# Optimization experiments

Hardware: AMD Instinct MI355X
Metric: run time of the kernel (lower is better)

The kernel has to match this reference:

```python
import math
import jax, jax.numpy as jnp
import numpy as np


def _cirlen(scale):
    # replicates UpSample.get_cirlen: smallest rational period of the scale
    for i in (10, 100, 1000, 10000):
        y = scale * i
        x = i
        if y == math.floor(y):
            break
    y = int(round(y))
    g = math.gcd(x, y)
    return y // g


def _proj(out_len, scale, scale_int, in_len):
    # replicates matmask_made: for each output coord, source coord and repeat index (sca),
    # giving the selected column p = coord*scale_int + sca in the nearest-repeated grid.
    c = np.arange(out_len, dtype=np.float64)
    c[-1] -= 0.1
    coord = np.floor(c / scale).astype(np.int64)
    sca = np.arange(out_len) - np.searchsorted(coord, coord)  # occurrence index per coord
    p = coord * scale_int + sca
    # unfold(kernel=3, dilation=2, padding=2): taps at p-2, p, p+2 in the upscaled grid
    q = p[:, None] + 2 * np.array([-1, 0, 1], dtype=np.int64)[None, :]
    valid = ((q >= 0) & (q < in_len * scale_int)).astype(np.float32)
    src = np.clip(q // scale_int, 0, in_len - 1)  # upscaled pixel q == original pixel q//scale_int
    return src, valid


def reference(x, w1, b1, w2, b2, ln_g, ln_b, scale_x10):
    scale = round(scale_x10 / 10.0, 4)
    scale_int = math.ceil(scale)
    N, C, H, W = x.shape
    outH = math.ceil(scale * H)
    outW = math.ceil(scale * W)
    cycle = _cirlen(scale)
    K = 9 * C

    # ---- per-cycle-position dynamic weights (Scale2Pos_mat + Fea2Weight + LayerNorm) ----
    off = np.arange(cycle, dtype=np.float64) / scale
    off = (off - np.floor(off)).astype(np.float32)
    oh_i, ow_j = np.meshgrid(off, off, indexing='ij')  # row index = i*cycle + j
    posmat = np.stack([np.full_like(oh_i, 1.0 / scale), oh_i, ow_j], axis=-1).reshape(-1, 3)
    posmat = jnp.asarray(posmat)
    h = jax.nn.relu(posmat @ w1 + b1)                       # (cyc^2, 256)
    wflat = h @ w2 + b2                                     # (cyc^2, 9*C*outC)
    outC = wflat.shape[-1] // K
    wv = wflat.reshape(cycle * cycle, outC, K)              # view(pos, outC, K)
    mu = wv.mean(-1, keepdims=True)
    var = wv.var(-1, keepdims=True)                         # biased, as torch LayerNorm
    wv = ((wv - mu) / jnp.sqrt(var + 1e-5)) * ln_g + ln_b
    wv = wv / C
    Wm = jnp.transpose(wv, (0, 2, 1)).reshape(cycle, cycle, K, outC)

    # ---- irregular gather (nearest-repeat + unfold + mask_select), done as direct gather ----
    rs, vh = _proj(outH, scale, scale_int, H)  # (outH,3)
    cs, vw = _proj(outW, scale, scale_int, W)  # (outW,3)
    g = x[:, :, jnp.asarray(rs), :]            # (N,C,outH,3,W)
    g = g[:, :, :, :, jnp.asarray(cs)]         # (N,C,outH,3,outW,3)
    g = g * jnp.asarray(vh)[None, None, :, :, None, None]
    g = g * jnp.asarray(vw)[None, None, None, None, :, :]
    # unfold channel order is (C, kh, kw)
    patch = jnp.transpose(g, (0, 2, 4, 1, 3, 5)).reshape(N, outH, outW, K)

    # ---- pad to cycle multiple, per-cycle-position matmul, crop ----
    Hp = -(-outH // cycle) * cycle
    Wp = -(-outW // cycle) * cycle
    patch = jnp.pad(patch, ((0, 0), (0, Hp - outH), (0, Wp - outW), (0, 0)))
    patch = patch.reshape(N, Hp // cycle, cycle, Wp // cycle, cycle, K)
    out = jnp.einsum('nhiwjk,ijkc->nchiwj', patch, Wm)
    out = out.reshape(N, outC, Hp, Wp)[:, :, :outH, :outW]
    return out


def setup_inputs() -> dict:
    key = jax.random.key(0)
    k = jax.random.split(key, 5)
    inC, outC = 64, 3
    x = jax.random.normal(k[0], (8, inC, 96, 96), dtype=jnp.float32)
    w1 = jax.random.normal(k[1], (3, 256), dtype=jnp.float32) * 0.5
    b1 = jax.random.normal(k[2], (256,), dtype=jnp.float32) * 0.1
    w2 = jax.random.normal(k[3], (256, 9 * inC * outC), dtype=jnp.float32) * 0.0625
    b2 = jax.random.normal(k[4], (9 * inC * outC,), dtype=jnp.float32) * 0.01
    ln_g = jnp.ones((9 * inC,), dtype=jnp.float32)
    ln_b = jnp.zeros((9 * inC,), dtype=jnp.float32)
    return {"x": x, "w1": w1, "b1": b1, "w2": w2, "b2": b2,
            "ln_g": ln_g, "ln_b": ln_b, "scale_x10": 15}
```

## Files before the change

### kernel.cpp

```cpp
#include <hip/hip_runtime.h>
#include <math.h>

#define C_IN   64
#define HW_IN  96
#define N_B    8
#define OUTC   3
#define OUT_HW 144
#define HID    256
#define KDIM   576
#define NFLAT  1728

typedef __attribute__((ext_vector_type(8))) short short8;
typedef __attribute__((ext_vector_type(4))) float f32x4;

#define XP_BYTES   (8u * 98 * 98 * 64 * 2)
#define WP_OFF     XP_BYTES
#define WF_OFF     (WP_OFF + 9 * 9216 * 2)
#define WS_NEED    (WF_OFF + NFLAT * 9 * 4)

#define WS_W    0
#define WS_RS   15552
#define WS_VH   15984
#define WS_WF   16416

__device__ __forceinline__ short f2bf(float f) {
    unsigned u = __float_as_uint(f);
    u += 0x7FFFu + ((u >> 16) & 1u);
    return (short)(u >> 16);
}

__global__ __launch_bounds__(256) void a1_wflat(
    const float* __restrict__ w1, const float* __restrict__ b1,
    const float* __restrict__ w2, const float* __restrict__ b2,
    const int* __restrict__ sxp, float* __restrict__ wf)
{
    __shared__ float h[HID];
    __shared__ float part[4 * 64];
    const int cell = blockIdx.x;
    const int tile = blockIdx.y;
    const int tid  = threadIdx.x;

    double scale = (double)sxp[0] / 10.0;
    int ci = cell / 3, cj = cell % 3;
    double oi = (double)ci / scale; oi -= floor(oi);
    double oj = (double)cj / scale; oj -= floor(oj);
    float p0 = (float)(1.0 / scale), p1 = (float)oi, p2 = (float)oj;

    float hv = b1[tid] + p0 * w1[tid] + p1 * w1[HID + tid] + p2 * w1[2 * HID + tid];
    h[tid] = fmaxf(hv, 0.f);
    __syncthreads();

    const int wave = tid >> 6, lane = tid & 63;
    const int col  = tile * 64 + lane;
    const float* w2c = w2 + (size_t)(wave * 64) * NFLAT + col;
    const float* hp  = h + wave * 64;
    float v = 0.f;
    #pragma unroll
    for (int r = 0; r < 64; ++r) v += hp[r] * w2c[(size_t)r * NFLAT];
    part[wave * 64 + lane] = v;
    __syncthreads();

    if (tid < 64) {
        int c2 = tile * 64 + tid;
        float s = b2[c2] + part[tid] + part[64 + tid] + part[128 + tid] + part[192 + tid];
        wf[cell * NFLAT + c2] = s;
    }
}

__global__ __launch_bounds__(128) void prep_xp(
    const float* __restrict__ x, short* __restrict__ xp)
{
    const int n = blockIdx.x, rp = blockIdx.y, sp = threadIdx.x;
    if (sp >= 98) return;
    short8* dst = (short8*)(xp + (((size_t)n * 98 + rp) * 98 + sp) * 64);
    const bool border = (rp == 0) | (rp == 97) | (sp == 0) | (sp == 97);
    if (border) {
        short8 z = {0, 0, 0, 0, 0, 0, 0, 0};
        #pragma unroll
        for (int q = 0; q < 8; ++q) dst[q] = z;
    } else {
        const float* xs = x + (size_t)n * C_IN * 9216 + (rp - 1) * 96 + (sp - 1);
        #pragma unroll
        for (int q = 0; q < 8; ++q) {
            short8 v;
            #pragma unroll
            for (int e = 0; e < 8; ++e)
                v[e] = f2bf(xs[(size_t)(q * 8 + e) * 9216]);
            dst[q] = v;
        }
    }
}

__global__ __launch_bounds__(256) void a2_lnW(
    const float* __restrict__ ln_g, const float* __restrict__ ln_b,
    const float* __restrict__ wf, short* __restrict__ Wp)
{
    __shared__ float rsum[4], rsum2[4];
    const int cell = blockIdx.x, co = blockIdx.y, tid = threadIdx.x;
    const int lane = tid & 63, wid = tid >> 6;

    const float* wfc = wf + cell * NFLAT + co * KDIM;

    float s = 0.f, s2 = 0.f;
    for (int k = tid; k < KDIM; k += 256) { float v = wfc[k]; s += v; s2 += v * v; }
    #pragma unroll
    for (int off = 32; off > 0; off >>= 1) { s += __shfl_down(s, off); s2 += __shfl_down(s2, off); }
    if (lane == 0) { rsum[wid] = s; rsum2[wid] = s2; }
    __syncthreads();
    float S  = rsum[0] + rsum[1] + rsum[2] + rsum[3];
    float Q  = rsum2[0] + rsum2[1] + rsum2[2] + rsum2[3];
    float mu = S * (1.f / KDIM);
    float rstd = rsqrtf(Q * (1.f / KDIM) - mu * mu + 1e-5f);

    for (int k = tid; k < KDIM; k += 256) {
        float v = ((wfc[k] - mu) * rstd * ln_g[k] + ln_b[k]) * (1.f / C_IN);
        int c = k / 9, t = k - 9 * c;
        int kp = t * 64 + c;
        Wp[((size_t)(cell * 72 + (kp >> 3)) * 16 + co) * 8 + (kp & 7)] = f2bf(v);
    }
    if (co == 0) {
        for (int e = tid; e < 72 * 13 * 8; e += 256) {
            int u = e & 7, r = e >> 3;
            int colz = 3 + (r % 13), kc = r / 13;
            Wp[((size_t)(cell * 72 + kc) * 16 + colz) * 8 + u] = 0;
        }
    }
}

__global__ __launch_bounds__(256) void c_mfma(
    const short* __restrict__ xp, const short* __restrict__ Wp,
    float* __restrict__ out)
{
    __shared__ short Bs[9216];
    const int tid = threadIdx.x;
    const int phase = blockIdx.y;
    const int i = phase / 3, jj = phase % 3;

    {
        short8* d = (short8*)Bs;
        const short8* sgl = (const short8*)(Wp + (size_t)phase * 9216);
        for (int e = tid; e < 1152; e += 256) d[e] = sgl[e];
    }
    __syncthreads();

    const int lane = tid & 63, wave = tid >> 6;
    const int q = lane >> 4;

    const int pix = blockIdx.x * 64 + wave * 16;
    const int m0 = pix % 48;
    const int t2 = pix / 48;
    const int k  = t2 % 48;
    const int n  = t2 / 48;

    const int di = (i == 2), dj = (jj == 2);
    const int r0 = 2 * k + di;
    const int m  = m0 + (lane & 15);
    const int s0 = 2 * m + dj;

    const short8* A0 = (const short8*)(xp + (((size_t)n * 98 + r0) * 98 + s0) * 64 + q * 8);
    const short8* A1 = A0 + 98 * 8;
    const short8* A2 = A0 + 196 * 8;
    const short8* Bp = (const short8*)Bs + (q * 16 + (lane & 15));

    f32x4 acc = {0.f, 0.f, 0.f, 0.f};
    #pragma unroll
    for (int kb = 0; kb < 18; ++kb) {
        const int t = kb >> 1, dr = t / 3, dc = t % 3;
        short8 av = (dr == 0 ? A0 : dr == 1 ? A1 : A2)[dc * 8 + (kb & 1) * 4];
        short8 bv = Bp[kb * 64];
        acc = __builtin_amdgcn_mfma_f32_16x16x32_bf16(av, bv, acc, 0, 0, 0);
    }

    const int col = lane & 15;
    if (col < 3) {
        const int oh = i + 3 * k;
        const size_t ob = ((size_t)(n * OUTC + col) * OUT_HW + oh) * OUT_HW;
        #pragma unroll
        for (int reg = 0; reg < 4; ++reg) {
            int mm = m0 + q * 4 + reg;
            out[ob + jj + 3 * mm] = acc[reg];
        }
    }
}

__global__ __launch_bounds__(256) void a2_ln_pack_proj(
    const float* __restrict__ ln_g, const float* __restrict__ ln_b,
    const int* __restrict__ sxp, float* __restrict__ ws)
{
    __shared__ float rsum[4], rsum2[4];
    const int cell = blockIdx.x, co = blockIdx.y, tid = threadIdx.x;
    const int lane = tid & 63, wid = tid >> 6;

    const float* wfc = ws + WS_WF + cell * NFLAT + co * KDIM;

    float s = 0.f, s2 = 0.f;
    for (int k = tid; k < KDIM; k += 256) { float v = wfc[k]; s += v; s2 += v * v; }
    #pragma unroll
    for (int off = 32; off > 0; off >>= 1) { s += __shfl_down(s, off); s2 += __shfl_down(s2, off); }
    if (lane == 0) { rsum[wid] = s; rsum2[wid] = s2; }
    __syncthreads();
    float S  = rsum[0] + rsum[1] + rsum[2] + rsum[3];
    float Q  = rsum2[0] + rsum2[1] + rsum2[2] + rsum2[3];
    float mu = S * (1.f / KDIM);
    float rstd = rsqrtf(Q * (1.f / KDIM) - mu * mu + 1e-5f);

    for (int k = tid; k < KDIM; k += 256) {
        float v = ((wfc[k] - mu) * rstd * ln_g[k] + ln_b[k]) * (1.f / C_IN);
        int c = k / 9, t = k % 9;
        ws[WS_W + cell * NFLAT + c * 27 + t * 3 + co] = v;
    }

    if (cell == 0 && co == 0 && tid < OUT_HW) {
        double scale = (double)sxp[0] / 10.0;
        int scale_int = (int)ceil(scale - 1e-9);
        double cc = (double)tid; if (tid == OUT_HW - 1) cc -= 0.1;
        long coord = (long)floor(cc / scale);
        long first = (long)ceil((double)coord * scale);
        long p = coord * (long)scale_int + ((long)tid - first);
        #pragma unroll
        for (int d = 0; d < 3; ++d) {
            long qq = p + 2 * (d - 1);
            bool ok = (qq >= 0) && (qq < (long)HW_IN * scale_int);
            long src = (qq < 0) ? 0 : qq / scale_int;
            if (src > HW_IN - 1) src = HW_IN - 1;
            ws[WS_RS + tid * 3 + d] = (float)src;
            ws[WS_VH + tid * 3 + d] = ok ? 1.f : 0.f;
        }
    }
}

#define JSTRIDE 2056
__global__ __launch_bounds__(192) void c_main(
    const float* __restrict__ x, const float* __restrict__ ws,
    float* __restrict__ out)
{
    __shared__ float Wl[3 * JSTRIDE];
    const int tid = threadIdx.x;
    const int oh  = blockIdx.x;
    const int n   = blockIdx.y;
    const int i   = oh % 3;

    for (int idx = tid; idx < 3 * 64 * 32; idx += 192) {
        int j = idx >> 11;
        int rem = idx & 2047;
        int c = rem >> 5, mm = rem & 31;
        float v = 0.f;
        if (mm < 27) v = ws[WS_W + (size_t)((i * 3 + j) * 64 + c) * 27 + mm];
        Wl[j * JSTRIDE + c * 32 + mm] = v;
    }
    __syncthreads();

    const int ow = tid;
    if (ow >= OUT_HW) return;

    const float* rsf = ws + WS_RS;
    const float* vhf = ws + WS_VH;
    const int jjf = ow % 3;
    const float* Wj = Wl + jjf * JSTRIDE;

    int s[3]; float vw[3];
    #pragma unroll
    for (int d = 0; d < 3; ++d) { s[d] = (int)rsf[ow * 3 + d]; vw[d] = vhf[ow * 3 + d]; }

    int xoff[9]; float vv[9];
    #pragma unroll
    for (int dr = 0; dr < 3; ++dr) {
        int r = (int)rsf[oh * 3 + dr];
        float vhd = vhf[oh * 3 + dr];
        #pragma unroll
        for (int dc = 0; dc < 3; ++dc) {
            xoff[dr * 3 + dc] = r * HW_IN + s[dc];
            vv[dr * 3 + dc]   = vhd * vw[dc];
        }
    }

    const float* xb = x + (size_t)n * C_IN * HW_IN * HW_IN;
    float acc[3] = {0.f, 0.f, 0.f};

    #pragma unroll 2
    for (int c = 0; c < C_IN; ++c) {
        const float* xc = xb + c * (HW_IN * HW_IN);
        float w[28];
        const float4* wp = (const float4*)(Wj + c * 32);
        #pragma unroll
        for (int qq = 0; qq < 7; ++qq) ((float4*)w)[qq] = wp[qq];
        #pragma unroll
        for (int t = 0; t < 9; ++t) {
            float xv = xc[xoff[t]] * vv[t];
            acc[0] += xv * w[t * 3 + 0];
            acc[1] += xv * w[t * 3 + 1];
            acc[2] += xv * w[t * 3 + 2];
        }
    }

    #pragma unroll
    for (int co = 0; co < OUTC; ++co)
        out[((size_t)(n * OUTC + co) * OUT_HW + oh) * OUT_HW + ow] = acc[co];
}

extern "C" void kernel_launch(void* const* d_in, const int* in_sizes, int n_in,
                              void* d_out, int out_size, void* d_ws, size_t ws_size,
                              hipStream_t stream)
{
    const float* x    = (const float*)d_in[0];
    const float* w1   = (const float*)d_in[1];
    const float* b1   = (const float*)d_in[2];
    const float* w2   = (const float*)d_in[3];
    const float* b2   = (const float*)d_in[4];
    const float* ln_g = (const float*)d_in[5];
    const float* ln_b = (const float*)d_in[6];
    const int*   sx   = (const int*)d_in[7];
    float* out = (float*)d_out;
    char*  wsb = (char*)d_ws;

    if (ws_size >= (size_t)WS_NEED) {
        short* xp = (short*)wsb;
        short* Wp = (short*)(wsb + WP_OFF);
        float* wf = (float*)(wsb + WF_OFF);
        a1_wflat<<<dim3(9, 27), 256, 0, stream>>>(w1, b1, w2, b2, sx, wf);
        prep_xp<<<dim3(8, 98), 128, 0, stream>>>(x, xp);
        a2_lnW<<<dim3(9, 3), 256, 0, stream>>>(ln_g, ln_b, wf, Wp);
        c_mfma<<<dim3(288, 9), 256, 0, stream>>>(xp, Wp, out);
    } else {
        float* ws = (float*)d_ws;
        a1_wflat<<<dim3(9, 27), 256, 0, stream>>>(w1, b1, w2, b2, sx, ws + WS_WF);
        a2_ln_pack_proj<<<dim3(9, 3), 256, 0, stream>>>(ln_g, ln_b, sx, ws);
        c_main<<<dim3(OUT_HW, N_B), 192, 0, stream>>>(x, ws, out);
    }
}
```

Measured before the change: 118.7 us.

## Fuse weight-generation MLP with LayerNorm packing and enlarge MFMA blocks

Merges the hidden-layer matmul kernel and the LayerNorm/bf16 packing kernel into a single kernel. Each block computes one (cell, output-channel) row of 576 weights, reduces its statistics in shared memory and writes the packed weights directly. This removes one launch and the intermediate wf buffer round trip. The main MFMA kernel now uses 512-thread blocks with two 16-pixel groups per wave, so each loaded B fragment is reused across two MFMAs and the grid has four times fewer blocks. The fused weight kernel has only 27 blocks, each doing a serial 256-step dot product per thread, which may lengthen the critical path.

```diff
diff --git a/kernel.cpp b/kernel.cpp
--- a/kernel.cpp
+++ b/kernel.cpp
@@ -15,8 +15,7 @@
 
 #define XP_BYTES   (8u * 98 * 98 * 64 * 2)
 #define WP_OFF     XP_BYTES
-#define WF_OFF     (WP_OFF + 9 * 9216 * 2)
-#define WS_NEED    (WF_OFF + NFLAT * 9 * 4)
+#define WS_NEED    (WP_OFF + 9 * 9216 * 2)
 
 #define WS_W    0
 #define WS_RS   15552
@@ -27,44 +26,6 @@
     unsigned u = __float_as_uint(f);
     u += 0x7FFFu + ((u >> 16) & 1u);
     return (short)(u >> 16);
-}
-
-__global__ __launch_bounds__(256) void a1_wflat(
-    const float* __restrict__ w1, const float* __restrict__ b1,
-    const float* __restrict__ w2, const float* __restrict__ b2,
-    const int* __restrict__ sxp, float* __restrict__ wf)
-{
-    __shared__ float h[HID];
-    __shared__ float part[4 * 64];
-    const int cell = blockIdx.x;
-    const int tile = blockIdx.y;
-    const int tid  = threadIdx.x;
-
-    double scale = (double)sxp[0] / 10.0;
-    int ci = cell / 3, cj = cell % 3;
-    double oi = (double)ci / scale; oi -= floor(oi);
-    double oj = (double)cj / scale; oj -= floor(oj);
-    float p0 = (float)(1.0 / scale), p1 = (float)oi, p2 = (float)oj;
-
-    float hv = b1[tid] + p0 * w1[tid] + p1 * w1[HID + tid] + p2 * w1[2 * HID + tid];
-    h[tid] = fmaxf(hv, 0.f);
-    __syncthreads();
-
-    const int wave = tid >> 6, lane = tid & 63;
-    const int col  = tile * 64 + lane;
-    const float* w2c = w2 + (size_t)(wave * 64) * NFLAT + col;
-    const float* hp  = h + wave * 64;
-    float v = 0.f;
-    #pragma unroll
-    for (int r = 0; r < 64; ++r) v += hp[r] * w2c[(size_t)r * NFLAT];
-    part[wave * 64 + lane] = v;
-    __syncthreads();
-
-    if (tid < 64) {
-        int c2 = tile * 64 + tid;
-        float s = b2[c2] + part[tid] + part[64 + tid] + part[128 + tid] + part[192 + tid];
-        wf[cell * NFLAT + c2] = s;
-    }
 }
 
 __global__ __launch_bounds__(128) void prep_xp(
@@ -91,35 +52,57 @@
     }
 }
 
-__global__ __launch_bounds__(256) void a2_lnW(
+__global__ __launch_bounds__(576) void ab_w(
+    const float* __restrict__ w1, const float* __restrict__ b1,
+    const float* __restrict__ w2, const float* __restrict__ b2,
     const float* __restrict__ ln_g, const float* __restrict__ ln_b,
-    const float* __restrict__ wf, short* __restrict__ Wp)
-{
-    __shared__ float rsum[4], rsum2[4];
+    const int* __restrict__ sxp, short* __restrict__ Wp)
+{
+    __shared__ float h[HID];
+    __shared__ float rs[9], rq[9], stat[2];
     const int cell = blockIdx.x, co = blockIdx.y, tid = threadIdx.x;
     const int lane = tid & 63, wid = tid >> 6;
 
-    const float* wfc = wf + cell * NFLAT + co * KDIM;
-
-    float s = 0.f, s2 = 0.f;
-    for (int k = tid; k < KDIM; k += 256) { float v = wfc[k]; s += v; s2 += v * v; }
+    if (tid < HID) {
+        double scale = (double)sxp[0] / 10.0;
+        int ci = cell / 3, cj = cell % 3;
+        double oi = (double)ci / scale; oi -= floor(oi);
+        double oj = (double)cj / scale; oj -= floor(oj);
+        float hv = b1[tid] + (float)(1.0 / scale) * w1[tid]
+                 + (float)oi * w1[HID + tid] + (float)oj * w1[2 * HID + tid];
+        h[tid] = fmaxf(hv, 0.f);
+    }
+    __syncthreads();
+
+    const int k = tid;
+    const int gcol = co * KDIM + k;
+    float v = b2[gcol];
+    const float* w2c = w2 + gcol;
+    #pragma unroll 32
+    for (int p = 0; p < HID; ++p) v += h[p] * w2c[(size_t)p * NFLAT];
+
+    float s = v, s2 = v * v;
     #pragma unroll
     for (int off = 32; off > 0; off >>= 1) { s += __shfl_down(s, off); s2 += __shfl_down(s2, off); }
-    if (lane == 0) { rsum[wid] = s; rsum2[wid] = s2; }
-    __syncthreads();
-    float S  = rsum[0] + rsum[1] + rsum[2] + rsum[3];
-    float Q  = rsum2[0] + rsum2[1] + rsum2[2] + rsum2[3];
-    float mu = S * (1.f / KDIM);
-    float rstd = rsqrtf(Q * (1.f / KDIM) - mu * mu + 1e-5f);
-
-    for (int k = tid; k < KDIM; k += 256) {
-        float v = ((wfc[k] - mu) * rstd * ln_g[k] + ln_b[k]) * (1.f / C_IN);
-        int c = k / 9, t = k - 9 * c;
-        int kp = t * 64 + c;
-        Wp[((size_t)(cell * 72 + (kp >> 3)) * 16 + co) * 8 + (kp & 7)] = f2bf(v);
-    }
+    if (lane == 0) { rs[wid] = s; rq[wid] = s2; }
+    __syncthreads();
+    if (tid == 0) {
+        float S = 0.f, Q = 0.f;
+        #pragma unroll
+        for (int w = 0; w < 9; ++w) { S += rs[w]; Q += rq[w]; }
+        float mu = S * (1.f / KDIM);
+        stat[0] = mu;
+        stat[1] = rsqrtf(Q * (1.f / KDIM) - mu * mu + 1e-5f);
+    }
+    __syncthreads();
+
+    float val = ((v - stat[0]) * stat[1] * ln_g[k] + ln_b[k]) * (1.f / C_IN);
+    int c = k / 9, t = k - 9 * c;
+    int kp = t * 64 + c;
+    Wp[((size_t)(cell * 72 + (kp >> 3)) * 16 + co) * 8 + (kp & 7)] = f2bf(val);
+
     if (co == 0) {
-        for (int e = tid; e < 72 * 13 * 8; e += 256) {
+        for (int e = tid; e < 72 * 13 * 8; e += 576) {
             int u = e & 7, r = e >> 3;
             int colz = 3 + (r % 13), kc = r / 13;
             Wp[((size_t)(cell * 72 + kc) * 16 + colz) * 8 + u] = 0;
@@ -127,7 +110,7 @@
     }
 }
 
-__global__ __launch_bounds__(256) void c_mfma(
+__global__ __launch_bounds__(512) void c_mfma(
     const short* __restrict__ xp, const short* __restrict__ Wp,
     float* __restrict__ out)
 {
@@ -138,48 +121,88 @@
 
     {
         short8* d = (short8*)Bs;
-        const short8* sgl = (const short8*)(Wp + (size_t)phase * 9216);
-        for (int e = tid; e < 1152; e += 256) d[e] = sgl[e];
+        const short8* sg = (const short8*)(Wp + (size_t)phase * 9216);
+        for (int e = tid; e < 1152; e += 512) d[e] = sg[e];
     }
     __syncthreads();
 
     const int lane = tid & 63, wave = tid >> 6;
-    const int q = lane >> 4;
-
-    const int pix = blockIdx.x * 64 + wave * 16;
-    const int m0 = pix % 48;
-    const int t2 = pix / 48;
-    const int k  = t2 % 48;
-    const int n  = t2 / 48;
-
+    const int q = lane >> 4, col = lane & 15;
     const int di = (i == 2), dj = (jj == 2);
-    const int r0 = 2 * k + di;
-    const int m  = m0 + (lane & 15);
-    const int s0 = 2 * m + dj;
-
-    const short8* A0 = (const short8*)(xp + (((size_t)n * 98 + r0) * 98 + s0) * 64 + q * 8);
-    const short8* A1 = A0 + 98 * 8;
-    const short8* A2 = A0 + 196 * 8;
-    const short8* Bp = (const short8*)Bs + (q * 16 + (lane & 15));
-
-    f32x4 acc = {0.f, 0.f, 0.f, 0.f};
+    const short8* xpv = (const short8*)xp;
+    const short8* Bp  = (const short8*)Bs + (q * 16 + col);
+
+    int base[2], kk[2], m0[2], nn[2];
+    #pragma unroll
+    for (int g = 0; g < 2; ++g) {
+        int pix = blockIdx.x * 256 + wave * 32 + g * 16;
+        m0[g] = pix % 48;
+        int t2 = pix / 48;
+        kk[g] = t2 % 48;
+        nn[g] = t2 / 48;
+        int r0 = 2 * kk[g] + di;
+        int s0 = 2 * (m0[g] + col) + dj;
+        base[g] = ((nn[g] * 98 + r0) * 98 + s0) * 8 + q;
+    }
+
+    f32x4 acc0 = {0.f, 0.f, 0.f, 0.f}, acc1 = {0.f, 0.f, 0.f, 0.f};
     #pragma unroll
     for (int kb = 0; kb < 18; ++kb) {
-        const int t = kb >> 1, dr = t / 3, dc = t % 3;
-        short8 av = (dr == 0 ? A0 : dr == 1 ? A1 : A2)[dc * 8 + (kb & 1) * 4];
-        short8 bv = Bp[kb * 64];
-        acc = __builtin_amdgcn_mfma_f32_16x16x32_bf16(av, bv, acc, 0, 0, 0);
-    }
-
-    const int col = lane & 15;
+        const int t = kb >> 1, dr = t / 3, dc = t - 3 * dr;
+        const int off = (dr * 98 + dc) * 8 + (kb & 1) * 4;
+        short8 bv  = Bp[kb * 64];
+        short8 av0 = xpv[base[0] + off];
+        short8 av1 = xpv[base[1] + off];
+        acc0 = __builtin_amdgcn_mfma_f32_16x16x32_bf16(av0, bv, acc0, 0, 0, 0);
+        acc1 = __builtin_amdgcn_mfma_f32_16x16x32_bf16(av1, bv, acc1, 0, 0, 0);
+    }
+
     if (col < 3) {
-        const int oh = i + 3 * k;
-        const size_t ob = ((size_t)(n * OUTC + col) * OUT_HW + oh) * OUT_HW;
-        #pragma unroll
-        for (int reg = 0; reg < 4; ++reg) {
-            int mm = m0 + q * 4 + reg;
-            out[ob + jj + 3 * mm] = acc[reg];
-        }
+        #pragma unroll
+        for (int g = 0; g < 2; ++g) {
+            const f32x4 a = g ? acc1 : acc0;
+            const int oh = i + 3 * kk[g];
+            const size_t ob = ((size_t)(nn[g] * OUTC + col) * OUT_HW + oh) * OUT_HW + jj;
+            #pragma unroll
+            for (int reg = 0; reg < 4; ++reg)
+                out[ob + 3 * (m0[g] + q * 4 + reg)] = a[reg];
+        }
+    }
+}
+
+__global__ __launch_bounds__(256) void a1_wflat(
+    const float* __restrict__ w1, const float* __restrict__ b1,
+    const float* __restrict__ w2, const float* __restrict__ b2,
+    const int* __restrict__ sxp, float* __restrict__ wf)
+{
+    __shared__ float h[HID];
+    __shared__ float part[4 * 64];
+    const int cell = blockIdx.x, tile = blockIdx.y, tid = threadIdx.x;
+
+    double scale = (double)sxp[0] / 10.0;
+    int ci = cell / 3, cj = cell % 3;
+    double oi = (double)ci / scale; oi -= floor(oi);
+    double oj = (double)cj / scale; oj -= floor(oj);
+    float p0 = (float)(1.0 / scale), p1 = (float)oi, p2 = (float)oj;
+
+    float hv = b1[tid] + p0 * w1[tid] + p1 * w1[HID + tid] + p2 * w1[2 * HID + tid];
+    h[tid] = fmaxf(hv, 0.f);
+    __syncthreads();
+
+    const int wave = tid >> 6, lane = tid & 63;
+    const int col  = tile * 64 + lane;
+    const float* w2c = w2 + (size_t)(wave * 64) * NFLAT + col;
+    const float* hp  = h + wave * 64;
+    float v = 0.f;
+    #pragma unroll
+    for (int r = 0; r < 64; ++r) v += hp[r] * w2c[(size_t)r * NFLAT];
+    part[wave * 64 + lane] = v;
+    __syncthreads();
+
+    if (tid < 64) {
+        int c2 = tile * 64 + tid;
+        float s = b2[c2] + part[tid] + part[64 + tid] + part[128 + tid] + part[192 + tid];
+        wf[cell * NFLAT + c2] = s;
     }
 }
 
@@ -316,11 +339,9 @@
     if (ws_size >= (size_t)WS_NEED) {
         short* xp = (short*)wsb;
         short* Wp = (short*)(wsb + WP_OFF);
-        float* wf = (float*)(wsb + WF_OFF);
-        a1_wflat<<<dim3(9, 27), 256, 0, stream>>>(w1, b1, w2, b2, sx, wf);
         prep_xp<<<dim3(8, 98), 128, 0, stream>>>(x, xp);
-        a2_lnW<<<dim3(9, 3), 256, 0, stream>>>(ln_g, ln_b, wf, Wp);
-        c_mfma<<<dim3(288, 9), 256, 0, stream>>>(xp, Wp, out);
+        ab_w<<<dim3(9, 3), 576, 0, stream>>>(w1, b1, w2, b2, ln_g, ln_b, sx, Wp);
+        c_mfma<<<dim3(72, 9), 512, 0, stream>>>(xp, Wp, out);
     } else {
         float* ws = (float*)d_ws;
         a1_wflat<<<dim3(9, 27), 256, 0, stream>>>(w1, b1, w2, b2, sx, ws + WS_WF);
```

Result: no change. 120.5 us (+1.5%).
